# Performance work log

Measured on AMD Instinct MI355X. Metric: run time of the kernel, lower is better.

The kernel has to match this reference:

```python
import jax, jax.numpy as jnp
import numpy as np

MODES = (16, 16)

def setup_inputs() -> dict:
    key = jax.random.key(0)
    ks = jax.random.split(key, 8)
    B, Cin, Cout, H, W = 16, 64, 64, 128, 128
    scale = 1.0 / (Cin * Cout)
    return {
        "x": jax.random.normal(ks[0], (B, Cin, H, W), jnp.float32),
        "t_emb": jax.random.normal(ks[1], (B, 512), jnp.float32),
        "weight_real": jax.random.normal(ks[2], (Cin, Cout, *MODES), jnp.float32) * 2 * scale - scale,
        "weight_imag": jax.random.normal(ks[3], (Cin, Cout, *MODES), jnp.float32) * 2 * scale - scale,
        "bypass_w": jax.random.normal(ks[4], (Cout, Cin), jnp.float32) * 0.05,
        "bypass_b": jax.random.normal(ks[5], (Cout,), jnp.float32) * 0.05,
        "temb_w": jax.random.normal(ks[6], (Cin, 512), jnp.float32) * 0.02,
        "temb_b": jax.random.normal(ks[7], (Cin,), jnp.float32) * 0.02,
    }

def reference(x, t_emb, weight_real, weight_imag, bypass_w, bypass_b, temb_w, temb_b):
    mk, ml = MODES
    H, W = x.shape[-2:]
    xf = x.astype(jnp.float32)
    # truncated spectral conv: rfft2 (ortho), keep low-mode corner only
    x_fft = jnp.fft.rfftn(xf, axes=(-2, -1), norm="ortho")[:, :, :mk, :ml]
    weight = weight_real + 1j * weight_imag  # [i, o, k, l]
    out_fft = jnp.einsum("bikl,iokl->bokl", x_fft, weight)
    x_spec = jnp.fft.irfftn(out_fft, s=(H, W), axes=(-2, -1), norm="ortho")
    # 1x1 conv bypass
    byp = jnp.einsum("bihw,oi->bohw", xf, bypass_w) + bypass_b[None, :, None, None]
    out = jax.nn.gelu(x_spec + byp, approximate=False)
    # temb fusion: x + Linear(silu(temb))[:, :, None, None]
    silu_t = t_emb * jax.nn.sigmoid(t_emb)
    proj = silu_t @ temb_w.T + temb_b  # [B, C]
    out = out + proj[:, :, None, None]
    return out
```

## Files before the change

kernel.cpp:

```cpp
#include <hip/hip_runtime.h>
#include <cmath>

#define TWO_PI_128 0.04908738521234052f

typedef __attribute__((ext_vector_type(8))) short bf16x8;
typedef __attribute__((ext_vector_type(4))) float f32x4;

__device__ inline unsigned short f2bf(float v) {
  unsigned u = __float_as_uint(v);
  unsigned r = (u + 0x7FFFu + ((u >> 16) & 1u)) >> 16;
  return (unsigned short)r;
}

__global__ __launch_bounds__(256) void proj_kernel(
    const float* __restrict__ t_emb, const float* __restrict__ temb_w,
    const float* __restrict__ temb_b, float* __restrict__ proj) {
  __shared__ float s_silu[512];
  __shared__ float s_part[64][4];
  const int b = blockIdx.x;
  const int t = threadIdx.x;
  for (int j = t; j < 512; j += 256) {
    float v = t_emb[b * 512 + j];
    s_silu[j] = v / (1.f + __expf(-v));
  }
  __syncthreads();
  const int o = t >> 2, part = t & 3;
  const float* wrow = temb_w + o * 512 + part * 128;
  const float* srow = s_silu + part * 128;
  float acc = 0.f;
#pragma unroll 8
  for (int j = 0; j < 128; ++j) acc = fmaf(srow[j], wrow[j], acc);
  s_part[o][part] = acc;
  __syncthreads();
  if (part == 0) {
    proj[b * 64 + o] =
        s_part[o][0] + s_part[o][1] + s_part[o][2] + s_part[o][3] + temb_b[o];
  }
}

__global__ __launch_bounds__(256) void wtrans_kernel(
    const float* __restrict__ wr, const float* __restrict__ wi,
    float* __restrict__ wt_r, float* __restrict__ wt_i) {
  __shared__ float tile[32][33];
  const float* src = blockIdx.z ? wi : wr;
  float* dst = blockIdx.z ? wt_i : wt_r;
  const int kl0 = blockIdx.x * 32, io0 = blockIdx.y * 32;
  const int ty = threadIdx.x >> 3, tx = threadIdx.x & 7;
  float4 v = *(const float4*)(src + (size_t)(io0 + ty) * 256 + kl0 + 4 * tx);
  tile[ty][4 * tx + 0] = v.x;
  tile[ty][4 * tx + 1] = v.y;
  tile[ty][4 * tx + 2] = v.z;
  tile[ty][4 * tx + 3] = v.w;
  __syncthreads();
  float4 o;
  o.x = tile[4 * tx + 0][ty];
  o.y = tile[4 * tx + 1][ty];
  o.z = tile[4 * tx + 2][ty];
  o.w = tile[4 * tx + 3][ty];
  *(float4*)(dst + (size_t)(kl0 + ty) * 4096 + io0 + 4 * tx) = o;
}

__global__ __launch_bounds__(256) void fwd_dft_kernel(
    const float* __restrict__ x, float* __restrict__ xfr_t,
    float* __restrict__ xfi_t) {
  __shared__ unsigned short s_x1[32 * 136];
  __shared__ float s_red[8 * 256];
  const int t = threadIdx.x;
  const int plane = blockIdx.x;
  const int wv = t >> 6, lane = t & 63, l15 = lane & 15, quad = lane >> 4;

  union U8 {
    bf16x8 v;
    unsigned short u[8];
  };

  float dC, dS;
  sincosf(TWO_PI_128 * (float)l15, &dS, &dC);

  U8 a_re[4], a_im[4];
#pragma unroll
  for (int ks = 0; ks < 4; ++ks) {
    const int w0 = ks * 32 + quad * 8;
    float c, s;
    sincosf(TWO_PI_128 * (float)((l15 * w0) & 127), &s, &c);
#pragma unroll
    for (int j = 0; j < 8; ++j) {
      a_re[ks].u[j] = f2bf(c);
      a_im[ks].u[j] = f2bf(-s);
      float nc = c * dC - s * dS;
      s = s * dC + c * dS;
      c = nc;
    }
  }

  const float* xp = x + (size_t)plane * 16384;
  f32x4 acc[2][2];
#pragma unroll
  for (int mt = 0; mt < 2; ++mt)
#pragma unroll
    for (int nt = 0; nt < 2; ++nt) acc[mt][nt] = (f32x4){0.f, 0.f, 0.f, 0.f};

#pragma unroll
  for (int ks = 0; ks < 4; ++ks) {
#pragma unroll
    for (int nt = 0; nt < 2; ++nt) {
      const float* src =
          xp + (size_t)((wv * 2 + nt) * 16 + l15) * 128 + ks * 32 + quad * 8;
      float4 v0 = *(const float4*)src;
      float4 v1 = *(const float4*)(src + 4);
      U8 bx;
      bx.u[0] = f2bf(v0.x);
      bx.u[1] = f2bf(v0.y);
      bx.u[2] = f2bf(v0.z);
      bx.u[3] = f2bf(v0.w);
      bx.u[4] = f2bf(v1.x);
      bx.u[5] = f2bf(v1.y);
      bx.u[6] = f2bf(v1.z);
      bx.u[7] = f2bf(v1.w);
      acc[0][nt] = __builtin_amdgcn_mfma_f32_16x16x32_bf16(a_re[ks].v, bx.v,
                                                           acc[0][nt], 0, 0, 0);
      acc[1][nt] = __builtin_amdgcn_mfma_f32_16x16x32_bf16(a_im[ks].v, bx.v,
                                                           acc[1][nt], 0, 0, 0);
    }
  }

#pragma unroll
  for (int mt = 0; mt < 2; ++mt)
#pragma unroll
    for (int nt = 0; nt < 2; ++nt)
#pragma unroll
      for (int r = 0; r < 4; ++r)
        s_x1[(mt * 16 + quad * 4 + r) * 136 + (wv * 2 + nt) * 16 + l15] =
            f2bf(acc[mt][nt][r]);
  __syncthreads();

  f32x4 accre = (f32x4){0.f, 0.f, 0.f, 0.f};
  f32x4 accim = (f32x4){0.f, 0.f, 0.f, 0.f};
#pragma unroll
  for (int kl2 = 0; kl2 < 2; ++kl2) {
    const int ks2 = wv * 2 + kl2;
    const int hb = (ks2 & 3) * 32 + quad * 8;
    const int imh = ks2 >> 2;
    float c, s;
    sincosf(TWO_PI_128 * (float)((l15 * hb) & 127), &s, &c);
    U8 ar, ai;
#pragma unroll
    for (int j = 0; j < 8; ++j) {
      if (!imh) {
        ar.u[j] = f2bf(c);
        ai.u[j] = f2bf(-s);
      } else {
        ar.u[j] = f2bf(s);
        ai.u[j] = f2bf(c);
      }
      float nc = c * dC - s * dS;
      s = s * dC + c * dS;
      c = nc;
    }
    bf16x8 bfrag = *(const bf16x8*)(s_x1 + (imh * 16 + l15) * 136 + hb);
    accre =
        __builtin_amdgcn_mfma_f32_16x16x32_bf16(ar.v, bfrag, accre, 0, 0, 0);
    accim =
        __builtin_amdgcn_mfma_f32_16x16x32_bf16(ai.v, bfrag, accim, 0, 0, 0);
  }
  *(f32x4*)(s_red + (wv * 2) * 256 + lane * 4) = accre;
  *(f32x4*)(s_red + (wv * 2 + 1) * 256 + lane * 4) = accim;
  __syncthreads();

  const float re = s_red[t] + s_red[512 + t] + s_red[1024 + t] + s_red[1536 + t];
  const float im =
      s_red[256 + t] + s_red[768 + t] + s_red[1280 + t] + s_red[1792 + t];
  const int k = (t >> 6) * 4 + (t & 3), l = (t >> 2) & 15;
  xfr_t[(size_t)(k * 16 + l) * 1024 + plane] = re * 0.0078125f;
  xfi_t[(size_t)(k * 16 + l) * 1024 + plane] = im * 0.0078125f;
}

__global__ __launch_bounds__(256) void modemix_kernel(
    const float* __restrict__ xfr_t, const float* __restrict__ xfi_t,
    const float* __restrict__ wt_r, const float* __restrict__ wt_i,
    float* __restrict__ ofr, float* __restrict__ ofi) {
  __shared__ float s_xr[1024], s_xi[1024];
  __shared__ float s_wr[4096], s_wi[4096];
  const int kl = blockIdx.x;
  const int t = threadIdx.x;
  ((float4*)s_xr)[t] = ((const float4*)(xfr_t + (size_t)kl * 1024))[t];
  ((float4*)s_xi)[t] = ((const float4*)(xfi_t + (size_t)kl * 1024))[t];
  const float4* wrp = (const float4*)(wt_r + (size_t)kl * 4096);
  const float4* wip = (const float4*)(wt_i + (size_t)kl * 4096);
#pragma unroll
  for (int j = 0; j < 4; ++j) {
    ((float4*)s_wr)[t + 256 * j] = wrp[t + 256 * j];
    ((float4*)s_wi)[t + 256 * j] = wip[t + 256 * j];
  }
  __syncthreads();
  const int b0 = t >> 6;
  const int o = t & 63;
  float accr[4] = {0.f, 0.f, 0.f, 0.f};
  float acci[4] = {0.f, 0.f, 0.f, 0.f};
  for (int i = 0; i < 64; ++i) {
    float wrv = s_wr[i * 64 + o], wiv = s_wi[i * 64 + o];
#pragma unroll
    for (int j = 0; j < 4; ++j) {
      int b = b0 + 4 * j;
      float xr = s_xr[b * 64 + i], xi = s_xi[b * 64 + i];
      accr[j] = fmaf(xr, wrv, accr[j]);
      accr[j] = fmaf(-xi, wiv, accr[j]);
      acci[j] = fmaf(xr, wiv, acci[j]);
      acci[j] = fmaf(xi, wrv, acci[j]);
    }
  }
#pragma unroll
  for (int j = 0; j < 4; ++j) {
    int b = b0 + 4 * j;
    ofr[(size_t)(b * 64 + o) * 256 + kl] = accr[j];
    ofi[(size_t)(b * 64 + o) * 256 + kl] = acci[j];
  }
}

__global__ __launch_bounds__(256) void invh_kernel(
    const float* __restrict__ ofr, const float* __restrict__ ofi,
    uint4* __restrict__ Ybf) {
  __shared__ float s_fr[16 * 260], s_fi[16 * 260];
  __shared__ float2 s_tw[128];
  const int t = threadIdx.x;
  const int bid = blockIdx.x;
  const int b = bid >> 5, og = (bid >> 3) & 3, hg = bid & 7;
  if (t < 128) {
    float sv, cv;
    sincosf(TWO_PI_128 * (float)t, &sv, &cv);
    s_tw[t] = make_float2(cv, sv);
  }
#pragma unroll 4
  for (int pp = 0; pp < 16; ++pp) {
    s_fr[pp * 260 + t] = ofr[(size_t)(b * 64 + og * 16 + pp) * 256 + t];
    s_fi[pp * 260 + t] = ofi[(size_t)(b * 64 + og * 16 + pp) * 256 + t];
  }
  __syncthreads();
  const int ol = t & 15, hl = t >> 4;
  const int h = hg * 16 + hl;
  float yr[16], yi[16];
#pragma unroll
  for (int l = 0; l < 16; ++l) {
    yr[l] = 0.f;
    yi[l] = 0.f;
  }
  const float* FR = s_fr + ol * 260;
  const float* FI = s_fi + ol * 260;
  const float2 tw = s_tw[h];
  float ck = 1.f, sk = 0.f;
#pragma unroll 4
  for (int k = 0; k < 16; ++k) {
#pragma unroll
    for (int q = 0; q < 4; ++q) {
      float4 fr = *(const float4*)(FR + k * 16 + 4 * q);
      float4 fi = *(const float4*)(FI + k * 16 + 4 * q);
      int l = 4 * q;
      yr[l + 0] = fmaf(fr.x, ck, yr[l + 0]);
      yr[l + 0] = fmaf(-fi.x, sk, yr[l + 0]);
      yi[l + 0] = fmaf(fi.x, ck, yi[l + 0]);
      yi[l + 0] = fmaf(fr.x, sk, yi[l + 0]);
      yr[l + 1] = fmaf(fr.y, ck, yr[l + 1]);
      yr[l + 1] = fmaf(-fi.y, sk, yr[l + 1]);
      yi[l + 1] = fmaf(fi.y, ck, yi[l + 1]);
      yi[l + 1] = fmaf(fr.y, sk, yi[l + 1]);
      yr[l + 2] = fmaf(fr.z, ck, yr[l + 2]);
      yr[l + 2] = fmaf(-fi.z, sk, yr[l + 2]);
      yi[l + 2] = fmaf(fi.z, ck, yi[l + 2]);
      yi[l + 2] = fmaf(fr.z, sk, yi[l + 2]);
      yr[l + 3] = fmaf(fr.w, ck, yr[l + 3]);
      yr[l + 3] = fmaf(-fi.w, sk, yr[l + 3]);
      yi[l + 3] = fmaf(fi.w, ck, yi[l + 3]);
      yi[l + 3] = fmaf(fr.w, sk, yi[l + 3]);
    }
    float tt = sk * tw.y, uu = ck * tw.y;
    ck = fmaf(ck, tw.x, -tt);
    sk = fmaf(sk, tw.x, uu);
  }
  unsigned int u[16];
  {
    float sc[16];
    sc[0] = 0.0078125f;
#pragma unroll
    for (int l = 1; l < 16; ++l) sc[l] = 0.015625f;
#pragma unroll
    for (int j = 0; j < 8; ++j) {
      u[j] = (unsigned)f2bf(yr[2 * j] * sc[2 * j]) |
             ((unsigned)f2bf(yr[2 * j + 1] * sc[2 * j + 1]) << 16);
      u[8 + j] = (unsigned)f2bf(yi[2 * j] * sc[2 * j]) |
                 ((unsigned)f2bf(yi[2 * j + 1] * sc[2 * j + 1]) << 16);
    }
  }
  uint4* dst = Ybf + ((size_t)(b * 128 + h) * 64 + og * 16 + ol) * 4;
  dst[0] = make_uint4(u[0], u[1], u[2], u[3]);
  dst[1] = make_uint4(u[4], u[5], u[6], u[7]);
  dst[2] = make_uint4(u[8], u[9], u[10], u[11]);
  dst[3] = make_uint4(u[12], u[13], u[14], u[15]);
}

__global__ __launch_bounds__(256) void final_kernel(
    const float* __restrict__ x, const float* __restrict__ bw,
    const float* __restrict__ bb, const float* __restrict__ proj,
    const uint4* __restrict__ Ybf, float* __restrict__ out) {
#define AR 104
  __shared__ unsigned short s_A[64 * AR];
  __shared__ float s_bb[64];
  __shared__ float s_pb[64];
  const int h = blockIdx.x, b = blockIdx.y, t = threadIdx.x;

  if (t < 64)
    s_bb[t] = bb[t];
  else if (t < 128)
    s_pb[t - 64] = proj[b * 64 + (t - 64)];

  {
    const int o = t >> 2, q = t & 3;
    const float4* src = (const float4*)(bw + o * 64 + q * 16);
    unsigned int u[8];
#pragma unroll
    for (int m = 0; m < 4; ++m) {
      float4 v = src[m];
      u[2 * m] = (unsigned)f2bf(v.x) | ((unsigned)f2bf(v.y) << 16);
      u[2 * m + 1] = (unsigned)f2bf(v.z) | ((unsigned)f2bf(v.w) << 16);
    }
    uint4* dst = (uint4*)(s_A + o * AR + q * 16);
    dst[0] = make_uint4(u[0], u[1], u[2], u[3]);
    dst[1] = make_uint4(u[4], u[5], u[6], u[7]);
  }
  {
    const int o = t >> 2, q = t & 3;
    uint4 v = Ybf[((size_t)(b * 128 + h) * 64 + o) * 4 + q];
    *(uint4*)(s_A + o * AR + 64 + q * 8) = v;
  }
  __syncthreads();

  const int wv = t >> 6, lane = t & 63;
  const int l15 = lane & 15, quad = lane >> 4;
  const int n0w = wv * 32;

  f32x4 acc[4][2];
#pragma unroll
  for (int mt = 0; mt < 4; ++mt) {
    f32x4 bv = *(const f32x4*)(s_bb + mt * 16 + quad * 4);
    acc[mt][0] = bv;
    acc[mt][1] = bv;
  }

  const float* xrow = x + (size_t)b * 1048576 + (size_t)h * 128 + n0w + l15;
#pragma unroll
  for (int ks = 0; ks < 64; ks += 32) {
    union {
      bf16x8 v;
      unsigned short u[8];
    } bx[2];
#pragma unroll
    for (int nt = 0; nt < 2; ++nt) {
      float xv[8];
#pragma unroll
      for (int j = 0; j < 8; ++j)
        xv[j] = xrow[(size_t)(ks + quad * 8 + j) * 16384 + nt * 16];
#pragma unroll
      for (int j = 0; j < 8; ++j) bx[nt].u[j] = f2bf(xv[j]);
    }
#pragma unroll
    for (int mt = 0; mt < 4; ++mt) {
      bf16x8 a = *(const bf16x8*)(s_A + (mt * 16 + l15) * AR + ks + quad * 8);
      acc[mt][0] = __builtin_amdgcn_mfma_f32_16x16x32_bf16(a, bx[0].v,
                                                           acc[mt][0], 0, 0, 0);
      acc[mt][1] = __builtin_amdgcn_mfma_f32_16x16x32_bf16(a, bx[1].v,
                                                           acc[mt][1], 0, 0, 0);
    }
  }

  {
    const int lbase = (quad & 1) * 8;
    const bool iscos = (quad < 2);
    union {
      bf16x8 v;
      unsigned short u[8];
    } bs[2];
#pragma unroll
    for (int nt = 0; nt < 2; ++nt) {
      const int wn = n0w + nt * 16 + l15;
      float st, ct, ss, cc;
      sincosf(TWO_PI_128 * (float)wn, &st, &ct);
      sincosf(TWO_PI_128 * (float)(wn * lbase), &ss, &cc);
#pragma unroll
      for (int j = 0; j < 8; ++j) {
        bs[nt].u[j] = f2bf(iscos ? cc : -ss);
        float nc = cc * ct - ss * st;
        ss = ss * ct + cc * st;
        cc = nc;
      }
    }
#pragma unroll
    for (int mt = 0; mt < 4; ++mt) {
      bf16x8 a = *(const bf16x8*)(s_A + (mt * 16 + l15) * AR + 64 + quad * 8);
      acc[mt][0] = __builtin_amdgcn_mfma_f32_16x16x32_bf16(a, bs[0].v,
                                                           acc[mt][0], 0, 0, 0);
      acc[mt][1] = __builtin_amdgcn_mfma_f32_16x16x32_bf16(a, bs[1].v,
                                                           acc[mt][1], 0, 0, 0);
    }
  }

#pragma unroll
  for (int mt = 0; mt < 4; ++mt) {
    f32x4 pv = *(const f32x4*)(s_pb + mt * 16 + quad * 4);
#pragma unroll
    for (int nt = 0; nt < 2; ++nt) {
      const int wcol = n0w + nt * 16 + l15;
#pragma unroll
      for (int r = 0; r < 4; ++r) {
        const int o = mt * 16 + quad * 4 + r;
        float v = acc[mt][nt][r];
        float g = fmaf(0.5f * v, 1.f + erff(v * 0.70710678f), pv[r]);
        out[((size_t)(b * 64 + o) * 128 + h) * 128 + wcol] = g;
      }
    }
  }
#undef AR
}

extern "C" void kernel_launch(void* const* d_in, const int* in_sizes, int n_in,
                              void* d_out, int out_size, void* d_ws,
                              size_t ws_size, hipStream_t stream) {
  (void)in_sizes;
  (void)n_in;
  (void)out_size;
  (void)ws_size;
  const float* x = (const float*)d_in[0];
  const float* t_emb = (const float*)d_in[1];
  const float* wr = (const float*)d_in[2];
  const float* wi = (const float*)d_in[3];
  const float* bw = (const float*)d_in[4];
  const float* bb = (const float*)d_in[5];
  const float* tw = (const float*)d_in[6];
  const float* tb = (const float*)d_in[7];
  float* out = (float*)d_out;

  char* ws = (char*)d_ws;
  float* proj = (float*)(ws);
  float* ofr = (float*)(ws + ((size_t)1 << 20));
  float* ofi = (float*)(ws + ((size_t)2 << 20));
  float* xfr_t = (float*)(ws + ((size_t)3 << 20));
  float* xfi_t = (float*)(ws + ((size_t)4 << 20));
  float* wt_r = (float*)(ws + ((size_t)5 << 20));
  float* wt_i = (float*)(ws + ((size_t)9 << 20));
  uint4* Ybf = (uint4*)(ws + ((size_t)3 << 20));

  proj_kernel<<<16, 256, 0, stream>>>(t_emb, tw, tb, proj);
  wtrans_kernel<<<dim3(8, 128, 2), 256, 0, stream>>>(wr, wi, wt_r, wt_i);
  fwd_dft_kernel<<<1024, 256, 0, stream>>>(x, xfr_t, xfi_t);
  modemix_kernel<<<256, 256, 0, stream>>>(xfr_t, xfi_t, wt_r, wt_i, ofr, ofi);
  invh_kernel<<<512, 256, 0, stream>>>(ofr, ofi, Ybf);
  final_kernel<<<dim3(128, 16), 256, 0, stream>>>(x, bw, bb, proj, Ybf, out);
}
```

Baseline: 186.4 us.

## Merge proj, weight-transpose and forward DFT into one launch; widen modemix blocks

The three independent front kernels (temb projection, weight transpose, forward truncated DFT) become one launch that dispatches on block index, with shared memory unioned across the three roles. This removes two kernel launches and the serialization between them. Separately, the mode-mix kernel now uses 1024 threads per block, so each thread handles one batch element instead of four, and it keeps split accumulators that are combined at the end. That gives more parallelism per mode but less register reuse of the weight loads.

```diff
diff --git a/kernel.cpp b/kernel.cpp
--- a/kernel.cpp
+++ b/kernel.cpp
@@ -12,61 +12,74 @@
   return (unsigned short)r;
 }
 
-__global__ __launch_bounds__(256) void proj_kernel(
-    const float* __restrict__ t_emb, const float* __restrict__ temb_w,
-    const float* __restrict__ temb_b, float* __restrict__ proj) {
-  __shared__ float s_silu[512];
-  __shared__ float s_part[64][4];
-  const int b = blockIdx.x;
+__global__ __launch_bounds__(256) void front_kernel(
+    const float* __restrict__ x, float* __restrict__ xfr_t,
+    float* __restrict__ xfi_t, const float* __restrict__ wr,
+    const float* __restrict__ wi, float* __restrict__ wt_r,
+    float* __restrict__ wt_i, const float* __restrict__ t_emb,
+    const float* __restrict__ temb_w, const float* __restrict__ temb_b,
+    float* __restrict__ proj) {
+  __shared__ union SM {
+    struct {
+      unsigned short x1[32 * 136];
+      float red[8 * 256];
+    } f;
+    float tile[32][33];
+    struct {
+      float silu[512];
+      float part[64][4];
+    } p;
+  } sm;
+
+  const int bid = blockIdx.x;
   const int t = threadIdx.x;
-  for (int j = t; j < 512; j += 256) {
-    float v = t_emb[b * 512 + j];
-    s_silu[j] = v / (1.f + __expf(-v));
-  }
-  __syncthreads();
-  const int o = t >> 2, part = t & 3;
-  const float* wrow = temb_w + o * 512 + part * 128;
-  const float* srow = s_silu + part * 128;
-  float acc = 0.f;
+
+  if (bid >= 3072) {
+    const int b = bid - 3072;
+    for (int j = t; j < 512; j += 256) {
+      float v = t_emb[b * 512 + j];
+      sm.p.silu[j] = v / (1.f + __expf(-v));
+    }
+    __syncthreads();
+    const int o = t >> 2, part = t & 3;
+    const float* wrow = temb_w + o * 512 + part * 128;
+    const float* srow = sm.p.silu + part * 128;
+    float acc = 0.f;
 #pragma unroll 8
-  for (int j = 0; j < 128; ++j) acc = fmaf(srow[j], wrow[j], acc);
-  s_part[o][part] = acc;
-  __syncthreads();
-  if (part == 0) {
-    proj[b * 64 + o] =
-        s_part[o][0] + s_part[o][1] + s_part[o][2] + s_part[o][3] + temb_b[o];
-  }
-}
-
-__global__ __launch_bounds__(256) void wtrans_kernel(
-    const float* __restrict__ wr, const float* __restrict__ wi,
-    float* __restrict__ wt_r, float* __restrict__ wt_i) {
-  __shared__ float tile[32][33];
-  const float* src = blockIdx.z ? wi : wr;
-  float* dst = blockIdx.z ? wt_i : wt_r;
-  const int kl0 = blockIdx.x * 32, io0 = blockIdx.y * 32;
-  const int ty = threadIdx.x >> 3, tx = threadIdx.x & 7;
-  float4 v = *(const float4*)(src + (size_t)(io0 + ty) * 256 + kl0 + 4 * tx);
-  tile[ty][4 * tx + 0] = v.x;
-  tile[ty][4 * tx + 1] = v.y;
-  tile[ty][4 * tx + 2] = v.z;
-  tile[ty][4 * tx + 3] = v.w;
-  __syncthreads();
-  float4 o;
-  o.x = tile[4 * tx + 0][ty];
-  o.y = tile[4 * tx + 1][ty];
-  o.z = tile[4 * tx + 2][ty];
-  o.w = tile[4 * tx + 3][ty];
-  *(float4*)(dst + (size_t)(kl0 + ty) * 4096 + io0 + 4 * tx) = o;
-}
-
-__global__ __launch_bounds__(256) void fwd_dft_kernel(
-    const float* __restrict__ x, float* __restrict__ xfr_t,
-    float* __restrict__ xfi_t) {
-  __shared__ unsigned short s_x1[32 * 136];
-  __shared__ float s_red[8 * 256];
-  const int t = threadIdx.x;
-  const int plane = blockIdx.x;
+    for (int j = 0; j < 128; ++j) acc = fmaf(srow[j], wrow[j], acc);
+    sm.p.part[o][part] = acc;
+    __syncthreads();
+    if (part == 0) {
+      proj[b * 64 + o] = sm.p.part[o][0] + sm.p.part[o][1] + sm.p.part[o][2] +
+                         sm.p.part[o][3] + temb_b[o];
+    }
+    return;
+  }
+
+  if (bid >= 1024) {
+    const int flat = bid - 1024;
+    const int tensor = flat >> 10;
+    const int rem = flat & 1023;
+    const int io0 = (rem >> 3) * 32, kl0 = (rem & 7) * 32;
+    const float* src = tensor ? wi : wr;
+    float* dst = tensor ? wt_i : wt_r;
+    const int ty = t >> 3, tx = t & 7;
+    float4 v = *(const float4*)(src + (size_t)(io0 + ty) * 256 + kl0 + 4 * tx);
+    sm.tile[ty][4 * tx + 0] = v.x;
+    sm.tile[ty][4 * tx + 1] = v.y;
+    sm.tile[ty][4 * tx + 2] = v.z;
+    sm.tile[ty][4 * tx + 3] = v.w;
+    __syncthreads();
+    float4 o;
+    o.x = sm.tile[4 * tx + 0][ty];
+    o.y = sm.tile[4 * tx + 1][ty];
+    o.z = sm.tile[4 * tx + 2][ty];
+    o.w = sm.tile[4 * tx + 3][ty];
+    *(float4*)(dst + (size_t)(kl0 + ty) * 4096 + io0 + 4 * tx) = o;
+    return;
+  }
+
+  const int plane = bid;
   const int wv = t >> 6, lane = t & 63, l15 = lane & 15, quad = lane >> 4;
 
   union U8 {
@@ -130,7 +143,7 @@
     for (int nt = 0; nt < 2; ++nt)
 #pragma unroll
       for (int r = 0; r < 4; ++r)
-        s_x1[(mt * 16 + quad * 4 + r) * 136 + (wv * 2 + nt) * 16 + l15] =
+        sm.f.x1[(mt * 16 + quad * 4 + r) * 136 + (wv * 2 + nt) * 16 + l15] =
             f2bf(acc[mt][nt][r]);
   __syncthreads();
 
@@ -157,25 +170,26 @@
       s = s * dC + c * dS;
       c = nc;
     }
-    bf16x8 bfrag = *(const bf16x8*)(s_x1 + (imh * 16 + l15) * 136 + hb);
+    bf16x8 bfrag = *(const bf16x8*)(sm.f.x1 + (imh * 16 + l15) * 136 + hb);
     accre =
         __builtin_amdgcn_mfma_f32_16x16x32_bf16(ar.v, bfrag, accre, 0, 0, 0);
     accim =
         __builtin_amdgcn_mfma_f32_16x16x32_bf16(ai.v, bfrag, accim, 0, 0, 0);
   }
-  *(f32x4*)(s_red + (wv * 2) * 256 + lane * 4) = accre;
-  *(f32x4*)(s_red + (wv * 2 + 1) * 256 + lane * 4) = accim;
+  *(f32x4*)(sm.f.red + (wv * 2) * 256 + lane * 4) = accre;
+  *(f32x4*)(sm.f.red + (wv * 2 + 1) * 256 + lane * 4) = accim;
   __syncthreads();
 
-  const float re = s_red[t] + s_red[512 + t] + s_red[1024 + t] + s_red[1536 + t];
-  const float im =
-      s_red[256 + t] + s_red[768 + t] + s_red[1280 + t] + s_red[1792 + t];
+  const float re =
+      sm.f.red[t] + sm.f.red[512 + t] + sm.f.red[1024 + t] + sm.f.red[1536 + t];
+  const float im = sm.f.red[256 + t] + sm.f.red[768 + t] + sm.f.red[1280 + t] +
+                   sm.f.red[1792 + t];
   const int k = (t >> 6) * 4 + (t & 3), l = (t >> 2) & 15;
   xfr_t[(size_t)(k * 16 + l) * 1024 + plane] = re * 0.0078125f;
   xfi_t[(size_t)(k * 16 + l) * 1024 + plane] = im * 0.0078125f;
 }
 
-__global__ __launch_bounds__(256) void modemix_kernel(
+__global__ __launch_bounds__(1024) void modemix_kernel(
     const float* __restrict__ xfr_t, const float* __restrict__ xfi_t,
     const float* __restrict__ wt_r, const float* __restrict__ wt_i,
     float* __restrict__ ofr, float* __restrict__ ofi) {
@@ -183,38 +197,30 @@
   __shared__ float s_wr[4096], s_wi[4096];
   const int kl = blockIdx.x;
   const int t = threadIdx.x;
-  ((float4*)s_xr)[t] = ((const float4*)(xfr_t + (size_t)kl * 1024))[t];
-  ((float4*)s_xi)[t] = ((const float4*)(xfi_t + (size_t)kl * 1024))[t];
-  const float4* wrp = (const float4*)(wt_r + (size_t)kl * 4096);
-  const float4* wip = (const float4*)(wt_i + (size_t)kl * 4096);
-#pragma unroll
-  for (int j = 0; j < 4; ++j) {
-    ((float4*)s_wr)[t + 256 * j] = wrp[t + 256 * j];
-    ((float4*)s_wi)[t + 256 * j] = wip[t + 256 * j];
-  }
+  if (t < 256)
+    ((float4*)s_xr)[t] = ((const float4*)(xfr_t + (size_t)kl * 1024))[t];
+  else if (t < 512)
+    ((float4*)s_xi)[t - 256] =
+        ((const float4*)(xfi_t + (size_t)kl * 1024))[t - 256];
+  ((float4*)s_wr)[t] = ((const float4*)(wt_r + (size_t)kl * 4096))[t];
+  ((float4*)s_wi)[t] = ((const float4*)(wt_i + (size_t)kl * 4096))[t];
   __syncthreads();
-  const int b0 = t >> 6;
+  const int b = t >> 6;
   const int o = t & 63;
-  float accr[4] = {0.f, 0.f, 0.f, 0.f};
-  float acci[4] = {0.f, 0.f, 0.f, 0.f};
+  const float* xrp = s_xr + b * 64;
+  const float* xip = s_xi + b * 64;
+  float ar0 = 0.f, ar1 = 0.f, ai0 = 0.f, ai1 = 0.f;
+#pragma unroll 4
   for (int i = 0; i < 64; ++i) {
     float wrv = s_wr[i * 64 + o], wiv = s_wi[i * 64 + o];
-#pragma unroll
-    for (int j = 0; j < 4; ++j) {
-      int b = b0 + 4 * j;
-      float xr = s_xr[b * 64 + i], xi = s_xi[b * 64 + i];
-      accr[j] = fmaf(xr, wrv, accr[j]);
-      accr[j] = fmaf(-xi, wiv, accr[j]);
-      acci[j] = fmaf(xr, wiv, acci[j]);
-      acci[j] = fmaf(xi, wrv, acci[j]);
-    }
-  }
-#pragma unroll
-  for (int j = 0; j < 4; ++j) {
-    int b = b0 + 4 * j;
-    ofr[(size_t)(b * 64 + o) * 256 + kl] = accr[j];
-    ofi[(size_t)(b * 64 + o) * 256 + kl] = acci[j];
-  }
+    float xr = xrp[i], xi = xip[i];
+    ar0 = fmaf(xr, wrv, ar0);
+    ar1 = fmaf(xi, wiv, ar1);
+    ai0 = fmaf(xr, wiv, ai0);
+    ai1 = fmaf(xi, wrv, ai1);
+  }
+  ofr[(size_t)(b * 64 + o) * 256 + kl] = ar0 - ar1;
+  ofi[(size_t)(b * 64 + o) * 256 + kl] = ai0 + ai1;
 }
 
 __global__ __launch_bounds__(256) void invh_kernel(
@@ -447,10 +453,9 @@
   float* wt_i = (float*)(ws + ((size_t)9 << 20));
   uint4* Ybf = (uint4*)(ws + ((size_t)3 << 20));
 
-  proj_kernel<<<16, 256, 0, stream>>>(t_emb, tw, tb, proj);
-  wtrans_kernel<<<dim3(8, 128, 2), 256, 0, stream>>>(wr, wi, wt_r, wt_i);
-  fwd_dft_kernel<<<1024, 256, 0, stream>>>(x, xfr_t, xfi_t);
-  modemix_kernel<<<256, 256, 0, stream>>>(xfr_t, xfi_t, wt_r, wt_i, ofr, ofi);
+  front_kernel<<<3088, 256, 0, stream>>>(x, xfr_t, xfi_t, wr, wi, wt_r, wt_i,
+                                         t_emb, tw, tb, proj);
+  modemix_kernel<<<256, 1024, 0, stream>>>(xfr_t, xfi_t, wt_r, wt_i, ofr, ofi);
   invh_kernel<<<512, 256, 0, stream>>>(ofr, ofi, Ybf);
   final_kernel<<<dim3(128, 16), 256, 0, stream>>>(x, bw, bb, proj, Ybf, out);
 }
```

Measured after the change: 177.3 us. 4.9% less time.
